# Kernel tuning notes

Measured on AMD Instinct MI355X. Metric: run time of the kernel, lower is better.

Reference implementation:

```python
import jax, jax.numpy as jnp
import numpy as np

N = 50000; E = 800000; B = 500; L = 42
F_IN = 35; HEADS = 10; F_H = 35; F_G = 350
VOCAB = 26; EMB = 128; NF = 16; OUT_DIM = 128; K = 8
NEG_SLOPE = 0.2


def setup_inputs() -> dict:
    key = jax.random.key(0)
    ks = jax.random.split(key, 16)
    inp = {}
    inp['x'] = jax.random.normal(ks[0], (N, F_IN), jnp.float32)
    inp['edge_index'] = jax.random.randint(ks[1], (2, E), 0, N, dtype=jnp.int32)
    inp['batch'] = jnp.sort(jax.random.randint(ks[2], (N,), 0, B, dtype=jnp.int32))
    inp['target'] = jax.random.randint(ks[3], (B, L), 0, VOCAB, dtype=jnp.int32)
    # --- learned parameters ---
    inp['W_gat'] = jax.random.normal(ks[4], (F_IN, HEADS * F_H), jnp.float32) * 0.1
    inp['att_src'] = jax.random.normal(ks[5], (HEADS, F_H), jnp.float32) * 0.1
    inp['att_dst'] = jax.random.normal(ks[6], (HEADS, F_H), jnp.float32) * 0.1
    inp['b_gat'] = jnp.zeros((HEADS * F_H,), jnp.float32)
    inp['W_gcn'] = jax.random.normal(ks[7], (F_G, F_G), jnp.float32) * 0.05
    inp['b_gcn'] = jnp.zeros((F_G,), jnp.float32)
    inp['W_fcg1'] = jax.random.normal(ks[8], (2 * F_G, 1500), jnp.float32) * 0.03
    inp['b_fcg1'] = jnp.zeros((1500,), jnp.float32)
    inp['W_fcg2'] = jax.random.normal(ks[9], (1500, OUT_DIM), jnp.float32) * 0.03
    inp['b_fcg2'] = jnp.zeros((OUT_DIM,), jnp.float32)
    inp['emb_xt'] = jax.random.normal(ks[10], (VOCAB, EMB), jnp.float32) * 0.1
    inp['W_conv'] = jax.random.normal(ks[11], (NF, EMB, K), jnp.float32) * 0.05
    inp['b_conv'] = jnp.zeros((NF,), jnp.float32)
    inp['W_fcxt'] = jax.random.normal(ks[12], (NF * 35, OUT_DIM), jnp.float32) * 0.05
    inp['b_fcxt'] = jnp.zeros((OUT_DIM,), jnp.float32)
    inp['W_fc1'] = jax.random.normal(ks[13], (256, 512), jnp.float32) * 0.05
    inp['b_fc1'] = jnp.zeros((512,), jnp.float32)
    inp['W_out'] = jax.random.normal(ks[14], (512, 1), jnp.float32) * 0.05
    inp['b_out'] = jnp.zeros((1,), jnp.float32)
    return inp


def _add_self_loops(edge_index):
    loop = jnp.arange(N, dtype=edge_index.dtype)
    src = jnp.concatenate([edge_index[0], loop])
    dst = jnp.concatenate([edge_index[1], loop])
    return src, dst


def _gat_conv(x, src, dst, W, att_src, att_dst, b):
    # h: [N, H, C]
    h = (x @ W).reshape(N, HEADS, F_H)
    a_s = jnp.einsum('nhc,hc->nh', h, att_src)  # [N, H]
    a_d = jnp.einsum('nhc,hc->nh', h, att_dst)
    e = jax.nn.leaky_relu(a_s[src] + a_d[dst], NEG_SLOPE)  # [Etot, H]
    # segment softmax over incoming edges per destination node, per head
    m = jax.ops.segment_max(e, dst, num_segments=N)
    m = jnp.where(jnp.isfinite(m), m, 0.0)
    ex = jnp.exp(e - m[dst])
    den = jax.ops.segment_sum(ex, dst, num_segments=N)
    alpha = ex / (den[dst] + 1e-16)  # [Etot, H]
    out = jax.ops.segment_sum(h[src] * alpha[:, :, None], dst, num_segments=N)
    return out.reshape(N, HEADS * F_H) + b, alpha


def _gcn_conv(x, src, dst, W, b):
    deg = jax.ops.segment_sum(jnp.ones_like(dst, jnp.float32), dst, num_segments=N)
    dinv = jnp.where(deg > 0, deg ** -0.5, 0.0)
    norm = dinv[src] * dinv[dst]  # symmetric normalization
    h = x @ W
    return jax.ops.segment_sum(h[src] * norm[:, None], dst, num_segments=N) + b


def reference(x, edge_index, batch, target, W_gat, att_src, att_dst, b_gat,
              W_gcn, b_gcn, W_fcg1, b_fcg1, W_fcg2, b_fcg2, emb_xt,
              W_conv, b_conv, W_fcxt, b_fcxt, W_fc1, b_fc1, W_out, b_out):
    src, dst = _add_self_loops(edge_index)
    # --- graph branch ---
    xg, alpha = _gat_conv(x, src, dst, W_gat, att_src, att_dst, b_gat)
    xg = jax.nn.relu(xg)
    xg = jax.nn.relu(_gcn_conv(xg, src, dst, W_gcn, b_gcn))
    # global max + mean pool per graph
    gmax = jax.ops.segment_max(xg, batch, num_segments=B)
    gsum = jax.ops.segment_sum(xg, batch, num_segments=B)
    cnt = jax.ops.segment_sum(jnp.ones((N,), jnp.float32), batch, num_segments=B)
    gmean = gsum / jnp.maximum(cnt, 1.0)[:, None]
    xg = jnp.concatenate([gmax, gmean], axis=1)  # [B, 700]
    xg = jax.nn.relu(xg @ W_fcg1 + b_fcg1)
    xg = xg @ W_fcg2 + b_fcg2  # [B, 128] (dropout is identity in eval)
    # --- protein branch ---
    emb = emb_xt[target]                      # [B, L, 128]
    emb = jnp.transpose(emb, (0, 2, 1))       # [B, 128, L]
    conv = jax.lax.conv_general_dilated(
        emb, W_conv, window_strides=(1,), padding='VALID',
        dimension_numbers=('NCH', 'OIH', 'NCH'))  # [B, 16, 35]
    conv = conv + b_conv[None, :, None]
    xt = conv.reshape(B, NF * 35)
    xt = xt @ W_fcxt + b_fcxt                 # [B, 128]
    # --- fusion ---
    xc = jnp.concatenate([xg, xt], axis=1)    # [B, 256]
    xc = jax.nn.relu(xc @ W_fc1 + b_fc1)
    out = jax.nn.sigmoid(xc @ W_out + b_out)  # [B, 1]
    return out, alpha
```

## Files before the change

kernel.cpp:

```cpp
#include <hip/hip_runtime.h>
#include <math.h>

#define NN 50000
#define EE 800000
#define BB 500
#define LL 42
#define NHEAD 10
#define FH 35
#define FG 350
#define ETOT (EE + NN)
#define NCHUNK ((NN + 511) / 512)

#define KPAD 384
#define LDH2 352
#define MPAD 50048
#define MB2  512

typedef unsigned short ushort_t;
typedef __attribute__((ext_vector_type(8))) short short8v;
typedef __attribute__((ext_vector_type(4))) float float4v;

__device__ __forceinline__ float lrelu(float x) { return x > 0.f ? x : 0.2f * x; }

__device__ __forceinline__ ushort_t f2bf(float f) {
    unsigned int u = __float_as_uint(f);
    u += 0x7fffu + ((u >> 16) & 1u);
    return (ushort_t)(u >> 16);
}
__device__ __forceinline__ float bflo(unsigned u) { return __uint_as_float(u << 16); }
__device__ __forceinline__ float bfhi(unsigned u) { return __uint_as_float(u & 0xffff0000u); }
__device__ __forceinline__ unsigned packbf(float a, float b) {
    return (unsigned)f2bf(a) | ((unsigned)f2bf(b) << 16);
}

__device__ __forceinline__ void async_cp16(const void* g, void* l) {
    __builtin_amdgcn_global_load_lds((const __attribute__((address_space(1))) unsigned int*)g,
                                     (__attribute__((address_space(3))) unsigned int*)l, 16, 0, 0);
}

__global__ __launch_bounds__(256) void k_init(int* deg, int* cur) {
    int i = blockIdx.x * 256 + threadIdx.x;
    if (i < NN) { deg[i] = 1; cur[i] = 0; }
}

__global__ __launch_bounds__(256) void k_deg(const int* __restrict__ ei, int* deg) {
    int i = blockIdx.x * 256 + threadIdx.x;
    if (i < EE) atomicAdd(&deg[ei[EE + i]], 1);
}

__global__ __launch_bounds__(512) void k_scan1(const int* __restrict__ deg, int* part) {
    int i = blockIdx.x * 512 + threadIdx.x;
    int lane = threadIdx.x & 63, wv = threadIdx.x >> 6;
    int x = (i < NN) ? deg[i] : 0;
    #pragma unroll
    for (int d = 32; d; d >>= 1) x += __shfl_xor(x, d);
    __shared__ int wsum[8];
    if (lane == 0) wsum[wv] = x;
    __syncthreads();
    if (threadIdx.x == 0) {
        int s = 0;
        #pragma unroll
        for (int w = 0; w < 8; w++) s += wsum[w];
        part[blockIdx.x] = s;
    }
}

__global__ __launch_bounds__(64) void k_scan2(const int* __restrict__ part, int* pscan) {
    int l = threadIdx.x;
    int v0 = (l < NCHUNK) ? part[l] : 0;
    #pragma unroll
    for (int d = 1; d < 64; d <<= 1) { int t = __shfl_up(v0, d); if (l >= d) v0 += t; }
    int tot0 = __shfl(v0, 63);
    int v1 = (64 + l < NCHUNK) ? part[64 + l] : 0;
    #pragma unroll
    for (int d = 1; d < 64; d <<= 1) { int t = __shfl_up(v1, d); if (l >= d) v1 += t; }
    v1 += tot0;
    if (l < NCHUNK) pscan[l] = v0;
    if (64 + l < NCHUNK) pscan[64 + l] = v1;
}

__global__ __launch_bounds__(512) void k_scan3(const int* __restrict__ deg, const int* __restrict__ pscan,
                                               int* offs) {
    int i = blockIdx.x * 512 + threadIdx.x;
    int lane = threadIdx.x & 63, wv = threadIdx.x >> 6;
    int x = (i < NN) ? deg[i] : 0;
    int incl = x;
    #pragma unroll
    for (int d = 1; d < 64; d <<= 1) { int t = __shfl_up(incl, d); if (lane >= d) incl += t; }
    __shared__ int wtot[8];
    if (lane == 63) wtot[wv] = incl;
    __syncthreads();
    int woff = 0;
    for (int w = 0; w < wv; w++) woff += wtot[w];
    int base = (blockIdx.x == 0) ? 0 : pscan[blockIdx.x - 1];
    if (i < NN) offs[i] = base + woff + incl - x;
}

__global__ __launch_bounds__(256) void k_scatter(const int* __restrict__ ei, const int* __restrict__ offs,
                                                 int* cur, int* csr_src) {
    int i = blockIdx.x * 256 + threadIdx.x;
    if (i < EE) {
        int s = ei[i], d = ei[EE + i];
        int slot = atomicAdd(&cur[d], 1);
        csr_src[offs[d] + slot] = s;
    } else if (i < ETOT) {
        int v = i - EE;
        int slot = atomicAdd(&cur[v], 1);
        csr_src[offs[v] + slot] = v;
    }
}

__global__ __launch_bounds__(256) void k_dinv(const int* __restrict__ deg, float* dinv) {
    int i = blockIdx.x * 256 + threadIdx.x;
    if (i < NN) dinv[i] = rsqrtf((float)deg[i]);
}

__global__ __launch_bounds__(256) void k_prep_xf(const float* __restrict__ x, ushort_t* __restrict__ xfb) {
    int i = blockIdx.x * 256 + threadIdx.x;
    if (i >= NN * 40) return;
    int n = i / 40, c = i % 40;
    xfb[i] = (c < 35) ? f2bf(x[n * 35 + c]) : (ushort_t)0;
}

__global__ __launch_bounds__(256) void k_prep_att(const float* __restrict__ W_gat, const float* __restrict__ att_s,
                                                  const float* __restrict__ att_d,
                                                  float* __restrict__ wS, float* __restrict__ wD) {
    int i = blockIdx.x * 256 + threadIdx.x;
    if (i >= FG) return;
    int hd = i / 35, c = i % 35;
    float ss = 0.f, dd = 0.f;
    for (int cc = 0; cc < 35; cc++) {
        float w = W_gat[c * FG + hd * 35 + cc];
        ss += w * att_s[hd * 35 + cc];
        dd += w * att_d[hd * 35 + cc];
    }
    wS[i] = ss;
    wD[i] = dd;
}

__global__ __launch_bounds__(256) void k_prep_wbd(const float* __restrict__ W_gat, ushort_t* __restrict__ Wt) {
    int i = blockIdx.x * 256 + threadIdx.x;
    if (i >= KPAD * KPAD) return;
    int n = i / KPAD, k = i % KPAD;
    int hd = k / 36, cc = k % 36;
    float v = 0.f;
    if (n < FG && cc < 35 && hd == n / 35) v = W_gat[cc * FG + n];
    Wt[i] = f2bf(v);
}

__global__ __launch_bounds__(256) void k_prep_wgcn(const float* __restrict__ W, ushort_t* __restrict__ Wt) {
    int i = blockIdx.x * 256 + threadIdx.x;
    if (i >= KPAD * KPAD) return;
    int n = i / KPAD, k = i % KPAD;
    float v = (n < FG && k < FG) ? W[k * FG + n] : 0.f;
    Wt[i] = f2bf(v);
}

__global__ __launch_bounds__(256) void k_prep_w(const float* __restrict__ W, ushort_t* __restrict__ Wt,
                                                int K, int N, int KP, int NP) {
    int i = blockIdx.x * 256 + threadIdx.x;
    if (i >= KP * NP) return;
    int k = i / NP, n = i % NP;
    float v = (k < K && n < N) ? W[(size_t)k * N + n] : 0.f;
    Wt[(size_t)n * KP + k] = f2bf(v);
}

__global__ __launch_bounds__(256) void k_cast_pad(const float* __restrict__ src, ushort_t* __restrict__ dst,
                                                  int M, int K, int MP, int KP) {
    int i = blockIdx.x * 256 + threadIdx.x;
    if (i >= MP * KP) return;
    int r = i / KP, k = i % KP;
    dst[i] = (r < M && k < K) ? f2bf(src[(size_t)r * K + k]) : (ushort_t)0;
}

__global__ __launch_bounds__(256) void k_zero_tail(ushort_t* buf) {
    int i = blockIdx.x * 256 + threadIdx.x;
    int total = (MPAD - NN) * KPAD;
    if (i < total) buf[(size_t)NN * KPAD + i] = 0;
}

__global__ __launch_bounds__(256) void k_mfma(const ushort_t* __restrict__ A, const ushort_t* __restrict__ Bt,
                                              void* __restrict__ C, int M, int Nv, int ldc, int lda,
                                              int ksteps, const float* __restrict__ bias, int act, int bf16out,
                                              int bdiag, int nst) {
    __shared__ ushort_t As[128 * 64];
    __shared__ ushort_t Bs[64 * 64];
    int tid = threadIdx.x;
    int wid = tid >> 6, lane = tid & 63;
    int m0 = blockIdx.y * 128, n0 = blockIdx.x * 64;
    int wm0 = (wid >> 1) * 64, wn0 = (wid & 1) * 32;
    int srow = tid >> 3;
    int scol = (tid & 7) * 8;
    float4v acc[4][2] = {{{0.f,0.f,0.f,0.f},{0.f,0.f,0.f,0.f}},
                         {{0.f,0.f,0.f,0.f},{0.f,0.f,0.f,0.f}},
                         {{0.f,0.f,0.f,0.f},{0.f,0.f,0.f,0.f}},
                         {{0.f,0.f,0.f,0.f},{0.f,0.f,0.f,0.f}}};
    int a_off = (wm0 + (lane & 15)) * 64 + (lane >> 4) * 8;
    int b_off = (wn0 + (lane & 15)) * 64 + (lane >> 4) * 8;
    int ks0 = 0, ks1 = ksteps;
    if (bdiag) {
        int hlo = n0 / 35;
        int hhi = (n0 + 63) / 35; if (hhi > 9) hhi = 9;
        ks0 = (hlo * 36) >> 6;
        ks1 = (hhi * 36 + 36 + 63) >> 6;
    }
    for (int ks = ks0; ks < ks1; ks++) {
        int k0 = ks * 64;
        #pragma unroll
        for (int r = 0; r < 4; r++) {
            const ushort_t* g = A + (size_t)(m0 + r * 32 + srow) * lda + k0 + scol;
            async_cp16(g, As + (r * 256 + tid) * 8);
        }
        #pragma unroll
        for (int r = 0; r < 2; r++) {
            const ushort_t* g = Bt + (size_t)(n0 + r * 32 + srow) * lda + k0 + scol;
            async_cp16(g, Bs + (r * 256 + tid) * 8);
        }
        __syncthreads();
        #pragma unroll
        for (int kh = 0; kh < 2; kh++) {
            short8v b0 = *(const short8v*)&Bs[b_off + kh * 32];
            short8v b1 = *(const short8v*)&Bs[b_off + 16 * 64 + kh * 32];
            #pragma unroll
            for (int mi = 0; mi < 4; mi++) {
                short8v a = *(const short8v*)&As[a_off + mi * 16 * 64 + kh * 32];
                acc[mi][0] = __builtin_amdgcn_mfma_f32_16x16x32_bf16(a, b0, acc[mi][0], 0, 0, 0);
                acc[mi][1] = __builtin_amdgcn_mfma_f32_16x16x32_bf16(a, b1, acc[mi][1], 0, 0, 0);
            }
        }
        __syncthreads();
    }
    int lm = m0 + wm0 + (lane >> 4) * 4;
    int lc = n0 + wn0 + (lane & 15);
    #pragma unroll
    for (int mi = 0; mi < 4; mi++) {
        #pragma unroll
        for (int ni = 0; ni < 2; ni++) {
            int col = lc + ni * 16;
            if (col >= nst) continue;
            float bv = (bias != nullptr && col < Nv) ? bias[col] : 0.f;
            #pragma unroll
            for (int r = 0; r < 4; r++) {
                int row = lm + mi * 16 + r;
                if (row >= M) continue;
                float v = acc[mi][ni][r] + bv;
                if (act) v = fmaxf(v, 0.f);
                if (col >= Nv) v = 0.f;
                if (bf16out) ((ushort_t*)C)[(size_t)row * ldc + col] = f2bf(v);
                else         ((float*)C)[(size_t)row * ldc + col] = v;
            }
        }
    }
}

__global__ __launch_bounds__(256) void k_att2(const float* __restrict__ x, const float* __restrict__ wS,
                                              const float* __restrict__ wD, float* __restrict__ a_s,
                                              float* __restrict__ a_d) {
    int tid = blockIdx.x * 256 + threadIdx.x;
    if (tid >= NN * NHEAD) return;
    int n = tid / NHEAD, hd = tid % NHEAD;
    const float* xr = x + (size_t)n * 35;
    const float* ws = wS + hd * 35;
    const float* wd = wD + hd * 35;
    float as = 0.f, ad = 0.f;
    #pragma unroll
    for (int c = 0; c < 35; c++) { float v = xr[c]; as += v * ws[c]; ad += v * wd[c]; }
    a_s[tid] = as;
    a_d[tid] = ad;
}

__global__ __launch_bounds__(256) void k_gat_agg(const ushort_t* __restrict__ xfb, const float* __restrict__ a_s,
                                                 const float* __restrict__ a_d,
                                                 const int* __restrict__ csr_src,
                                                 const int* __restrict__ offs, const int* __restrict__ deg,
                                                 ushort_t* __restrict__ Zb, float* __restrict__ denArr) {
    int wid = (blockIdx.x * blockDim.x + threadIdx.x) >> 6;
    int lane = threadIdx.x & 63;
    if (wid >= NN) return;
    int o0 = offs[wid], d = deg[wid];
    bool mine = (lane < NHEAD);
    float adv = mine ? a_d[wid * NHEAD + lane] : 0.f;
    int h1 = lane / 18,          c1 = lane % 18;
    int h2 = (lane + 64) / 18,   c2 = (lane + 64) % 18;
    bool g3 = lane < 52;
    int h3 = g3 ? (lane + 128) / 18 : 0;
    int c3 = g3 ? (lane + 128) % 18 : 0;
    float den = 0.f;
    float a1l = 0.f, a1h = 0.f, a2l = 0.f, a2h = 0.f, a3l = 0.f, a3h = 0.f;
    const unsigned* x32 = (const unsigned*)xfb;
    int i = 0;
    for (; i + 2 <= d; i += 2) {
        int s0 = csr_src[o0 + i], s1 = csr_src[o0 + i + 1];
        const unsigned* x0 = x32 + (size_t)s0 * 20;
        const unsigned* x1 = x32 + (size_t)s1 * 20;
        float as0 = mine ? a_s[s0 * NHEAD + lane] : 0.f;
        float as1 = mine ? a_s[s1 * NHEAD + lane] : 0.f;
        unsigned u01 = x0[c1], u02 = x0[c2], u03 = x0[c3];
        unsigned u11 = x1[c1], u12 = x1[c2], u13 = x1[c3];
        float ex0 = __expf(lrelu(as0 + adv));
        float ex1 = __expf(lrelu(as1 + adv));
        den += ex0 + ex1;
        float e01 = __shfl(ex0, h1), e02 = __shfl(ex0, h2), e03 = __shfl(ex0, h3);
        float e11 = __shfl(ex1, h1), e12 = __shfl(ex1, h2), e13 = __shfl(ex1, h3);
        a1l += e01 * bflo(u01) + e11 * bflo(u11);
        a1h += e01 * bfhi(u01) + e11 * bfhi(u11);
        a2l += e02 * bflo(u02) + e12 * bflo(u12);
        a2h += e02 * bfhi(u02) + e12 * bfhi(u12);
        a3l += e03 * bflo(u03) + e13 * bflo(u13);
        a3h += e03 * bfhi(u03) + e13 * bfhi(u13);
    }
    for (; i < d; i++) {
        int s = csr_src[o0 + i];
        const unsigned* x0 = x32 + (size_t)s * 20;
        float as0 = mine ? a_s[s * NHEAD + lane] : 0.f;
        unsigned u01 = x0[c1], u02 = x0[c2], u03 = x0[c3];
        float ex0 = __expf(lrelu(as0 + adv));
        den += ex0;
        float e01 = __shfl(ex0, h1), e02 = __shfl(ex0, h2), e03 = __shfl(ex0, h3);
        a1l += e01 * bflo(u01);  a1h += e01 * bfhi(u01);
        a2l += e02 * bflo(u02);  a2h += e02 * bfhi(u02);
        a3l += e03 * bflo(u03);  a3h += e03 * bfhi(u03);
    }
    float rden = 1.f / (den + 1e-16f);
    if (mine) denArr[wid * NHEAD + lane] = den;
    float r1 = __shfl(rden, h1), r2 = __shfl(rden, h2), r3 = __shfl(rden, h3);
    unsigned* zr = (unsigned*)(Zb + (size_t)wid * KPAD);
    __builtin_nontemporal_store(packbf(a1l * r1, a1h * r1), &zr[lane]);
    __builtin_nontemporal_store(packbf(a2l * r2, a2h * r2), &zr[lane + 64]);
    __builtin_nontemporal_store(g3 ? packbf(a3l * r3, a3h * r3) : 0u, &zr[lane + 128]);
}

__global__ __launch_bounds__(256) void k_alpha(const int* __restrict__ ei, const float* __restrict__ a_s,
                                               const float* __restrict__ a_d, const float* __restrict__ den,
                                               float* __restrict__ alphaOut) {
    int i = blockIdx.x * 256 + threadIdx.x;
    if (i >= ETOT * NHEAD) return;
    int e = i / NHEAD, hd = i % NHEAD;
    int s, dst;
    if (e < EE) { s = ei[e]; dst = ei[EE + e]; }
    else { s = dst = e - EE; }
    float ex = __expf(lrelu(a_s[s * NHEAD + hd] + a_d[dst * NHEAD + hd]));
    __builtin_nontemporal_store(ex / (den[dst * NHEAD + hd] + 1e-16f), &alphaOut[i]);
}

__global__ __launch_bounds__(256) void k_gcn_agg(const ushort_t* __restrict__ h2b,
                                                 const int* __restrict__ csr_src,
                                                 const int* __restrict__ offs, const int* __restrict__ deg,
                                                 const float* __restrict__ dinv, const float* __restrict__ b_gcn,
                                                 float* __restrict__ xg2) {
    int wid = (blockIdx.x * blockDim.x + threadIdx.x) >> 6;
    int lane = threadIdx.x & 63;
    if (wid >= NN) return;
    int o0 = offs[wid], d = deg[wid];
    float wv = dinv[wid];
    bool g3 = lane < 48;
    int w3 = g3 ? (lane + 128) : 0;
    float aL0 = 0.f, aH0 = 0.f, aL1 = 0.f, aH1 = 0.f, aL2 = 0.f, aH2 = 0.f;
    const unsigned* h32 = (const unsigned*)h2b;
    int i = 0;
    for (; i + 2 <= d; i += 2) {
        int s0 = csr_src[o0 + i], s1 = csr_src[o0 + i + 1];
        float w0 = dinv[s0], w1 = dinv[s1];
        const unsigned* h0 = h32 + (size_t)s0 * (LDH2 / 2);
        const unsigned* h1 = h32 + (size_t)s1 * (LDH2 / 2);
        unsigned u00 = h0[lane], u01 = h0[lane + 64], u02 = h0[w3];
        unsigned u10 = h1[lane], u11 = h1[lane + 64], u12 = h1[w3];
        aL0 += w0 * bflo(u00) + w1 * bflo(u10);
        aH0 += w0 * bfhi(u00) + w1 * bfhi(u10);
        aL1 += w0 * bflo(u01) + w1 * bflo(u11);
        aH1 += w0 * bfhi(u01) + w1 * bfhi(u11);
        aL2 += w0 * bflo(u02) + w1 * bflo(u12);
        aH2 += w0 * bfhi(u02) + w1 * bfhi(u12);
    }
    for (; i < d; i++) {
        int s = csr_src[o0 + i];
        float ws = dinv[s];
        const unsigned* hr = h32 + (size_t)s * (LDH2 / 2);
        unsigned u0 = hr[lane], u1 = hr[lane + 64], u2 = hr[w3];
        aL0 += ws * bflo(u0);  aH0 += ws * bfhi(u0);
        aL1 += ws * bflo(u1);  aH1 += ws * bfhi(u1);
        aL2 += ws * bflo(u2);  aH2 += ws * bfhi(u2);
    }
    float* orow = xg2 + (size_t)wid * FG;
    {
        int f = 2 * lane;
        __builtin_nontemporal_store(fmaxf(wv * aL0 + b_gcn[f], 0.f), &orow[f]);
        __builtin_nontemporal_store(fmaxf(wv * aH0 + b_gcn[f + 1], 0.f), &orow[f + 1]);
    }
    {
        int f = 128 + 2 * lane;
        __builtin_nontemporal_store(fmaxf(wv * aL1 + b_gcn[f], 0.f), &orow[f]);
        __builtin_nontemporal_store(fmaxf(wv * aH1 + b_gcn[f + 1], 0.f), &orow[f + 1]);
    }
    {
        int f = 256 + 2 * lane;
        if (f < FG) {
            __builtin_nontemporal_store(fmaxf(wv * aL2 + b_gcn[f], 0.f), &orow[f]);
            __builtin_nontemporal_store(fmaxf(wv * aH2 + b_gcn[f + 1], 0.f), &orow[f + 1]);
        }
    }
}

__device__ __forceinline__ int lowerB(const int* a, int n, int key) {
    int lo = 0, hi = n;
    while (lo < hi) { int mid = (lo + hi) >> 1; if (a[mid] < key) lo = mid + 1; else hi = mid; }
    return lo;
}

__global__ __launch_bounds__(384) void k_pool(const float* __restrict__ xg2, const int* __restrict__ batch,
                                              float* __restrict__ pooled) {
    int g = blockIdx.x;
    int f = threadIdx.x;
    int s = lowerB(batch, NN, g);
    int e = lowerB(batch, NN, g + 1);
    if (f >= FG) return;
    float mx = -INFINITY, sm = 0.f;
    int n = s;
    for (; n + 4 <= e; n += 4) {
        float v0 = xg2[(size_t)(n + 0) * FG + f];
        float v1 = xg2[(size_t)(n + 1) * FG + f];
        float v2 = xg2[(size_t)(n + 2) * FG + f];
        float v3 = xg2[(size_t)(n + 3) * FG + f];
        mx = fmaxf(fmaxf(mx, v0), fmaxf(fmaxf(v1, v2), v3));
        sm += v0 + v1 + v2 + v3;
    }
    for (; n < e; n++) {
        float v = xg2[(size_t)n * FG + f];
        mx = fmaxf(mx, v);
        sm += v;
    }
    int cnt = e - s;
    pooled[g * 700 + f] = mx;
    pooled[g * 700 + FG + f] = sm / fmaxf((float)cnt, 1.f);
}

__global__ __launch_bounds__(256) void k_conv(const int* __restrict__ target, const float* __restrict__ emb,
                                              const float* __restrict__ Wc, const float* __restrict__ bc,
                                              float* __restrict__ xt) {
    __shared__ float embL[26 * 132];
    __shared__ float WL[16 * 8 * 128];
    __shared__ int   tgL[2 * LL];
    int tid = threadIdx.x;
    int b0 = blockIdx.x * 2;
    for (int i = tid; i < 26 * 128; i += 256) {
        int r = i >> 7, e = i & 127;
        embL[r * 132 + e] = emb[i];
    }
    for (int i = tid; i < 16384; i += 256) {
        int f = i >> 10, rem = i & 1023, k = rem >> 7, e = rem & 127;
        WL[i] = Wc[f * 1024 + e * 8 + k];
    }
    if (tid < 2 * LL) tgL[tid] = target[b0 * LL + tid];
    __syncthreads();
    #pragma unroll
    for (int pass = 0; pass < 2; pass++) {
        int r = tid + pass * 256;
        if (r >= 280) break;
        int bl = r / 140, rem = r % 140;
        int fq = rem / 35, t = rem % 35;
        const int* tg = &tgL[bl * LL];
        float ac0 = 0.f, ac1 = 0.f, ac2 = 0.f, ac3 = 0.f;
        for (int k = 0; k < 8; k++) {
            const float* er = &embL[tg[t + k] * 132];
            const float* w0 = &WL[((fq * 4 + 0) * 8 + k) * 128];
            const float* w1 = &WL[((fq * 4 + 1) * 8 + k) * 128];
            const float* w2 = &WL[((fq * 4 + 2) * 8 + k) * 128];
            const float* w3 = &WL[((fq * 4 + 3) * 8 + k) * 128];
            #pragma unroll 8
            for (int e = 0; e < 128; e += 4) {
                float4 a = *(const float4*)&er[e];
                float4 q0 = *(const float4*)&w0[e];
                float4 q1 = *(const float4*)&w1[e];
                float4 q2 = *(const float4*)&w2[e];
                float4 q3 = *(const float4*)&w3[e];
                ac0 += a.x * q0.x + a.y * q0.y + a.z * q0.z + a.w * q0.w;
                ac1 += a.x * q1.x + a.y * q1.y + a.z * q1.z + a.w * q1.w;
                ac2 += a.x * q2.x + a.y * q2.y + a.z * q2.z + a.w * q2.w;
                ac3 += a.x * q3.x + a.y * q3.y + a.z * q3.z + a.w * q3.w;
            }
        }
        int b = b0 + bl, fb = fq * 4;
        xt[b * 560 + (fb + 0) * 35 + t] = ac0 + bc[fb + 0];
        xt[b * 560 + (fb + 1) * 35 + t] = ac1 + bc[fb + 1];
        xt[b * 560 + (fb + 2) * 35 + t] = ac2 + bc[fb + 2];
        xt[b * 560 + (fb + 3) * 35 + t] = ac3 + bc[fb + 3];
    }
}

__global__ __launch_bounds__(256) void k_out(const float* __restrict__ f1, const float* __restrict__ W_out,
                                             const float* __restrict__ b_out, float* __restrict__ out) {
    int wid = (blockIdx.x * blockDim.x + threadIdx.x) >> 6;
    int lane = threadIdx.x & 63;
    if (wid >= BB) return;
    const float* xr = f1 + (size_t)wid * 512;
    float acc = 0.f;
    #pragma unroll
    for (int k = 0; k < 8; k++) acc += xr[lane + k * 64] * W_out[lane + k * 64];
    #pragma unroll
    for (int d = 32; d; d >>= 1) acc += __shfl_xor(acc, d);
    if (lane == 0) out[wid] = 1.f / (1.f + __expf(-(acc + b_out[0])));
}

extern "C" void kernel_launch(void* const* d_in, const int* in_sizes, int n_in,
                              void* d_out, int out_size, void* d_ws, size_t ws_size,
                              hipStream_t stream) {
    const float* x      = (const float*)d_in[0];
    const int*   ei     = (const int*)d_in[1];
    const int*   batch  = (const int*)d_in[2];
    const int*   target = (const int*)d_in[3];
    const float* W_gat  = (const float*)d_in[4];
    const float* att_s  = (const float*)d_in[5];
    const float* att_d  = (const float*)d_in[6];
    const float* b_gat  = (const float*)d_in[7];
    const float* W_gcn  = (const float*)d_in[8];
    const float* b_gcn  = (const float*)d_in[9];
    const float* W_fcg1 = (const float*)d_in[10];
    const float* b_fcg1 = (const float*)d_in[11];
    const float* W_fcg2 = (const float*)d_in[12];
    const float* b_fcg2 = (const float*)d_in[13];
    const float* embxt  = (const float*)d_in[14];
    const float* W_conv = (const float*)d_in[15];
    const float* b_conv = (const float*)d_in[16];
    const float* W_fcxt = (const float*)d_in[17];
    const float* b_fcxt = (const float*)d_in[18];
    const float* W_fc1  = (const float*)d_in[19];
    const float* b_fc1  = (const float*)d_in[20];
    const float* W_out  = (const float*)d_in[21];
    const float* b_out  = (const float*)d_in[22];

    float* out_sig  = (float*)d_out;
    float* alphaOut = (float*)d_out + BB;

    size_t o = 0;
    auto alloc = [&](size_t bytes) -> void* {
        o = (o + 255) & ~(size_t)255;
        void* p = (char*)d_ws + o;
        o += bytes;
        return p;
    };
    int*   deg     = (int*)alloc((size_t)NN * 4);
    int*   cur     = (int*)alloc((size_t)NN * 4);
    int*   offs    = (int*)alloc((size_t)NN * 4);
    int*   part    = (int*)alloc(128 * 4);
    int*   pscan   = (int*)alloc(128 * 4);
    int*   csr_src = (int*)alloc((size_t)ETOT * 4);
    float* dinv    = (float*)alloc((size_t)NN * 4);
    float* a_s     = (float*)alloc((size_t)NN * NHEAD * 4);
    float* a_d     = (float*)alloc((size_t)NN * NHEAD * 4);
    float* denArr  = (float*)alloc((size_t)NN * NHEAD * 4);
    ushort_t* xfb  = (ushort_t*)alloc((size_t)NN * 40 * 2);
    float* wS      = (float*)alloc((size_t)FG * 4);
    float* wD      = (float*)alloc((size_t)FG * 4);
    ushort_t* WtBD = (ushort_t*)alloc((size_t)KPAD * KPAD * 2);
    ushort_t* WtGC = (ushort_t*)alloc((size_t)KPAD * KPAD * 2);
    ushort_t* WtF1 = (ushort_t*)alloc((size_t)1536 * 704 * 2);
    ushort_t* WtF2 = (ushort_t*)alloc((size_t)128 * 1536 * 2);
    ushort_t* WtFX = (ushort_t*)alloc((size_t)128 * 576 * 2);
    ushort_t* WtFC = (ushort_t*)alloc((size_t)512 * 256 * 2);
    float* pooled  = (float*)alloc((size_t)BB * 700 * 4);
    ushort_t* pooledb = (ushort_t*)alloc((size_t)MB2 * 704 * 2);
    ushort_t* t1b  = (ushort_t*)alloc((size_t)MB2 * 1536 * 2);
    float* xt      = (float*)alloc((size_t)BB * 560 * 4);
    ushort_t* xtb  = (ushort_t*)alloc((size_t)MB2 * 576 * 2);
    ushort_t* xcb  = (ushort_t*)alloc((size_t)MB2 * 256 * 2);
    float* f1      = (float*)alloc((size_t)MB2 * 512 * 4);
    ushort_t* hb   = (ushort_t*)alloc((size_t)MPAD * KPAD * 2);
    char*  R2      = (char*)alloc((size_t)NN * FG * 4);
    ushort_t* xg1b = (ushort_t*)R2;
    float* xg2     = (float*)R2;
    (void)ws_size; (void)n_in; (void)in_sizes; (void)out_size;

    auto mfma = [&](const ushort_t* A, const ushort_t* Bt, void* C, const float* bias,
                    int M2, int Nv, int NP, int ldc, int KP, int act, int bf16out, int bdiag, int nst) {
        dim3 g(NP / 64, M2 / 128);
        k_mfma<<<g, 256, 0, stream>>>(A, Bt, C, M2, Nv, ldc, KP, KP / 64, bias, act, bf16out, bdiag, nst);
    };

    k_init<<<(NN + 255) / 256, 256, 0, stream>>>(deg, cur);
    k_deg<<<(EE + 255) / 256, 256, 0, stream>>>(ei, deg);
    k_scan1<<<NCHUNK, 512, 0, stream>>>(deg, part);
    k_scan2<<<1, 64, 0, stream>>>(part, pscan);
    k_scan3<<<NCHUNK, 512, 0, stream>>>(deg, pscan, offs);
    k_scatter<<<(ETOT + 255) / 256, 256, 0, stream>>>(ei, offs, cur, csr_src);
    k_dinv<<<(NN + 255) / 256, 256, 0, stream>>>(deg, dinv);

    k_prep_xf<<<(NN * 40 + 255) / 256, 256, 0, stream>>>(x, xfb);
    k_prep_att<<<2, 256, 0, stream>>>(W_gat, att_s, att_d, wS, wD);
    k_prep_wbd<<<(KPAD * KPAD + 255) / 256, 256, 0, stream>>>(W_gat, WtBD);
    k_prep_wgcn<<<(KPAD * KPAD + 255) / 256, 256, 0, stream>>>(W_gcn, WtGC);
    k_prep_w<<<(704 * 1536 + 255) / 256, 256, 0, stream>>>(W_fcg1, WtF1, 700, 1500, 704, 1536);
    k_prep_w<<<(1536 * 128 + 255) / 256, 256, 0, stream>>>(W_fcg2, WtF2, 1500, 128, 1536, 128);
    k_prep_w<<<(576 * 128 + 255) / 256, 256, 0, stream>>>(W_fcxt, WtFX, 560, 128, 576, 128);
    k_prep_w<<<(256 * 512 + 255) / 256, 256, 0, stream>>>(W_fc1, WtFC, 256, 512, 256, 512);
    k_zero_tail<<<((MPAD - NN) * KPAD + 255) / 256, 256, 0, stream>>>(hb);

    k_att2<<<(NN * NHEAD + 255) / 256, 256, 0, stream>>>(x, wS, wD, a_s, a_d);
    k_gat_agg<<<(NN + 3) / 4, 256, 0, stream>>>(xfb, a_s, a_d, csr_src, offs, deg, hb, denArr);
    k_alpha<<<(ETOT * NHEAD + 255) / 256, 256, 0, stream>>>(ei, a_s, a_d, denArr, alphaOut);
    mfma(hb, WtBD, xg1b, b_gat, MPAD, FG, KPAD, KPAD, KPAD, 1, 1, 1, KPAD);

    mfma(xg1b, WtGC, hb, nullptr, MPAD, FG, KPAD, LDH2, KPAD, 0, 1, 0, LDH2);
    k_gcn_agg<<<(NN + 3) / 4, 256, 0, stream>>>(hb, csr_src, offs, deg, dinv, b_gcn, xg2);

    k_pool<<<BB, 384, 0, stream>>>(xg2, batch, pooled);
    k_cast_pad<<<(MB2 * 704 + 255) / 256, 256, 0, stream>>>(pooled, pooledb, BB, 700, MB2, 704);
    mfma(pooledb, WtF1, t1b, b_fcg1, MB2, 1500, 1536, 1536, 704, 1, 1, 0, 1536);
    mfma(t1b, WtF2, xcb, b_fcg2, MB2, 128, 128, 256, 1536, 0, 1, 0, 128);
    k_conv<<<250, 256, 0, stream>>>(target, embxt, W_conv, b_conv, xt);
    k_cast_pad<<<(MB2 * 576 + 255) / 256, 256, 0, stream>>>(xt, xtb, BB, 560, MB2, 576);
    mfma(xtb, WtFX, xcb + 128, b_fcxt, MB2, 128, 128, 256, 576, 0, 1, 0, 128);
    mfma(xcb, WtFC, f1, b_fc1, MB2, 512, 512, 512, 256, 1, 0, 0, 512);
    k_out<<<(BB + 3) / 4, 256, 0, stream>>>(f1, W_out, b_out, out_sig);
}
```

Measured before the change: 605.0 us.

## Fuse node prep with attention scores, unroll aggregations, store GCN output as bf16

Merges the bf16 feature cast and the per-node attention-score computation into one kernel that reads x once. It also unrolls both edge-aggregation loops to four neighbours per step and shrinks their blocks to two waves. The GCN aggregation now writes bf16 instead of fp32, which halves the write traffic and the read traffic of the pooling kernel that follows. In exchange, the pooled max and mean inputs lose precision to bf16 rounding.

```diff
diff --git a/kernel.cpp b/kernel.cpp
--- a/kernel.cpp
+++ b/kernel.cpp
@@ -115,13 +115,6 @@
     if (i < NN) dinv[i] = rsqrtf((float)deg[i]);
 }
 
-__global__ __launch_bounds__(256) void k_prep_xf(const float* __restrict__ x, ushort_t* __restrict__ xfb) {
-    int i = blockIdx.x * 256 + threadIdx.x;
-    if (i >= NN * 40) return;
-    int n = i / 40, c = i % 40;
-    xfb[i] = (c < 35) ? f2bf(x[n * 35 + c]) : (ushort_t)0;
-}
-
 __global__ __launch_bounds__(256) void k_prep_att(const float* __restrict__ W_gat, const float* __restrict__ att_s,
                                                   const float* __restrict__ att_d,
                                                   float* __restrict__ wS, float* __restrict__ wD) {
@@ -136,6 +129,35 @@
     }
     wS[i] = ss;
     wD[i] = dd;
+}
+
+__global__ __launch_bounds__(256) void k_prep_node(const float* __restrict__ x, const float* __restrict__ wS,
+                                                   const float* __restrict__ wD, ushort_t* __restrict__ xfb,
+                                                   float* __restrict__ a_s, float* __restrict__ a_d) {
+    __shared__ float sw[FG], dw[FG];
+    int tid = threadIdx.x;
+    for (int i = tid; i < FG; i += 256) { sw[i] = wS[i]; dw[i] = wD[i]; }
+    __syncthreads();
+    int n = blockIdx.x * 256 + tid;
+    if (n >= NN) return;
+    float xr[35];
+    #pragma unroll
+    for (int c = 0; c < 35; c++) xr[c] = x[(size_t)n * 35 + c];
+    unsigned* xo = (unsigned*)(xfb + (size_t)n * 40);
+    #pragma unroll
+    for (int w = 0; w < 17; w++) xo[w] = packbf(xr[2 * w], xr[2 * w + 1]);
+    xo[17] = packbf(xr[34], 0.f);
+    xo[18] = 0u; xo[19] = 0u;
+    #pragma unroll
+    for (int hd = 0; hd < NHEAD; hd++) {
+        const float* ws = &sw[hd * 35];
+        const float* wd = &dw[hd * 35];
+        float as = 0.f, ad = 0.f;
+        #pragma unroll
+        for (int c = 0; c < 35; c++) { float v = xr[c]; as += v * ws[c]; ad += v * wd[c]; }
+        a_s[n * NHEAD + hd] = as;
+        a_d[n * NHEAD + hd] = ad;
+    }
 }
 
 __global__ __launch_bounds__(256) void k_prep_wbd(const float* __restrict__ W_gat, ushort_t* __restrict__ Wt) {
@@ -253,28 +275,12 @@
     }
 }
 
-__global__ __launch_bounds__(256) void k_att2(const float* __restrict__ x, const float* __restrict__ wS,
-                                              const float* __restrict__ wD, float* __restrict__ a_s,
-                                              float* __restrict__ a_d) {
-    int tid = blockIdx.x * 256 + threadIdx.x;
-    if (tid >= NN * NHEAD) return;
-    int n = tid / NHEAD, hd = tid % NHEAD;
-    const float* xr = x + (size_t)n * 35;
-    const float* ws = wS + hd * 35;
-    const float* wd = wD + hd * 35;
-    float as = 0.f, ad = 0.f;
-    #pragma unroll
-    for (int c = 0; c < 35; c++) { float v = xr[c]; as += v * ws[c]; ad += v * wd[c]; }
-    a_s[tid] = as;
-    a_d[tid] = ad;
-}
-
-__global__ __launch_bounds__(256) void k_gat_agg(const ushort_t* __restrict__ xfb, const float* __restrict__ a_s,
+__global__ __launch_bounds__(128) void k_gat_agg(const ushort_t* __restrict__ xfb, const float* __restrict__ a_s,
                                                  const float* __restrict__ a_d,
                                                  const int* __restrict__ csr_src,
                                                  const int* __restrict__ offs, const int* __restrict__ deg,
                                                  ushort_t* __restrict__ Zb, float* __restrict__ denArr) {
-    int wid = (blockIdx.x * blockDim.x + threadIdx.x) >> 6;
+    int wid = blockIdx.x * 2 + (threadIdx.x >> 6);
     int lane = threadIdx.x & 63;
     if (wid >= NN) return;
     int o0 = offs[wid], d = deg[wid];
@@ -289,25 +295,36 @@
     float a1l = 0.f, a1h = 0.f, a2l = 0.f, a2h = 0.f, a3l = 0.f, a3h = 0.f;
     const unsigned* x32 = (const unsigned*)xfb;
     int i = 0;
-    for (; i + 2 <= d; i += 2) {
-        int s0 = csr_src[o0 + i], s1 = csr_src[o0 + i + 1];
+    for (; i + 4 <= d; i += 4) {
+        int s0 = csr_src[o0 + i],     s1 = csr_src[o0 + i + 1];
+        int s2 = csr_src[o0 + i + 2], s3 = csr_src[o0 + i + 3];
         const unsigned* x0 = x32 + (size_t)s0 * 20;
         const unsigned* x1 = x32 + (size_t)s1 * 20;
+        const unsigned* x2 = x32 + (size_t)s2 * 20;
+        const unsigned* x3 = x32 + (size_t)s3 * 20;
         float as0 = mine ? a_s[s0 * NHEAD + lane] : 0.f;
         float as1 = mine ? a_s[s1 * NHEAD + lane] : 0.f;
+        float as2 = mine ? a_s[s2 * NHEAD + lane] : 0.f;
+        float as3 = mine ? a_s[s3 * NHEAD + lane] : 0.f;
         unsigned u01 = x0[c1], u02 = x0[c2], u03 = x0[c3];
         unsigned u11 = x1[c1], u12 = x1[c2], u13 = x1[c3];
+        unsigned u21 = x2[c1], u22 = x2[c2], u23 = x2[c3];
+        unsigned u31 = x3[c1], u32 = x3[c2], u33 = x3[c3];
         float ex0 = __expf(lrelu(as0 + adv));
         float ex1 = __expf(lrelu(as1 + adv));
-        den += ex0 + ex1;
+        float ex2 = __expf(lrelu(as2 + adv));
+        float ex3 = __expf(lrelu(as3 + adv));
+        den += (ex0 + ex1) + (ex2 + ex3);
         float e01 = __shfl(ex0, h1), e02 = __shfl(ex0, h2), e03 = __shfl(ex0, h3);
         float e11 = __shfl(ex1, h1), e12 = __shfl(ex1, h2), e13 = __shfl(ex1, h3);
-        a1l += e01 * bflo(u01) + e11 * bflo(u11);
-        a1h += e01 * bfhi(u01) + e11 * bfhi(u11);
-        a2l += e02 * bflo(u02) + e12 * bflo(u12);
-        a2h += e02 * bfhi(u02) + e12 * bfhi(u12);
-        a3l += e03 * bflo(u03) + e13 * bflo(u13);
-        a3h += e03 * bfhi(u03) + e13 * bfhi(u13);
+        float e21 = __shfl(ex2, h1), e22 = __shfl(ex2, h2), e23 = __shfl(ex2, h3);
+        float e31 = __shfl(ex3, h1), e32 = __shfl(ex3, h2), e33 = __shfl(ex3, h3);
+        a1l += e01 * bflo(u01) + e11 * bflo(u11) + e21 * bflo(u21) + e31 * bflo(u31);
+        a1h += e01 * bfhi(u01) + e11 * bfhi(u11) + e21 * bfhi(u21) + e31 * bfhi(u31);
+        a2l += e02 * bflo(u02) + e12 * bflo(u12) + e22 * bflo(u22) + e32 * bflo(u32);
+        a2h += e02 * bfhi(u02) + e12 * bfhi(u12) + e22 * bfhi(u22) + e32 * bfhi(u32);
+        a3l += e03 * bflo(u03) + e13 * bflo(u13) + e23 * bflo(u23) + e33 * bflo(u33);
+        a3h += e03 * bfhi(u03) + e13 * bfhi(u13) + e23 * bfhi(u23) + e33 * bfhi(u33);
     }
     for (; i < d; i++) {
         int s = csr_src[o0 + i];
@@ -343,12 +360,12 @@
     __builtin_nontemporal_store(ex / (den[dst * NHEAD + hd] + 1e-16f), &alphaOut[i]);
 }
 
-__global__ __launch_bounds__(256) void k_gcn_agg(const ushort_t* __restrict__ h2b,
+__global__ __launch_bounds__(128) void k_gcn_agg(const ushort_t* __restrict__ h2b,
                                                  const int* __restrict__ csr_src,
                                                  const int* __restrict__ offs, const int* __restrict__ deg,
                                                  const float* __restrict__ dinv, const float* __restrict__ b_gcn,
-                                                 float* __restrict__ xg2) {
-    int wid = (blockIdx.x * blockDim.x + threadIdx.x) >> 6;
+                                                 ushort_t* __restrict__ xg2b) {
+    int wid = blockIdx.x * 2 + (threadIdx.x >> 6);
     int lane = threadIdx.x & 63;
     if (wid >= NN) return;
     int o0 = offs[wid], d = deg[wid];
@@ -358,19 +375,24 @@
     float aL0 = 0.f, aH0 = 0.f, aL1 = 0.f, aH1 = 0.f, aL2 = 0.f, aH2 = 0.f;
     const unsigned* h32 = (const unsigned*)h2b;
     int i = 0;
-    for (; i + 2 <= d; i += 2) {
-        int s0 = csr_src[o0 + i], s1 = csr_src[o0 + i + 1];
-        float w0 = dinv[s0], w1 = dinv[s1];
+    for (; i + 4 <= d; i += 4) {
+        int s0 = csr_src[o0 + i],     s1 = csr_src[o0 + i + 1];
+        int s2 = csr_src[o0 + i + 2], s3 = csr_src[o0 + i + 3];
+        float q0 = dinv[s0], q1 = dinv[s1], q2 = dinv[s2], q3 = dinv[s3];
         const unsigned* h0 = h32 + (size_t)s0 * (LDH2 / 2);
         const unsigned* h1 = h32 + (size_t)s1 * (LDH2 / 2);
+        const unsigned* h2 = h32 + (size_t)s2 * (LDH2 / 2);
+        const unsigned* h3 = h32 + (size_t)s3 * (LDH2 / 2);
         unsigned u00 = h0[lane], u01 = h0[lane + 64], u02 = h0[w3];
         unsigned u10 = h1[lane], u11 = h1[lane + 64], u12 = h1[w3];
-        aL0 += w0 * bflo(u00) + w1 * bflo(u10);
-        aH0 += w0 * bfhi(u00) + w1 * bfhi(u10);
-        aL1 += w0 * bflo(u01) + w1 * bflo(u11);
-        aH1 += w0 * bfhi(u01) + w1 * bfhi(u11);
-        aL2 += w0 * bflo(u02) + w1 * bflo(u12);
-        aH2 += w0 * bfhi(u02) + w1 * bfhi(u12);
+        unsigned u20 = h2[lane], u21 = h2[lane + 64], u22 = h2[w3];
+        unsigned u30 = h3[lane], u31 = h3[lane + 64], u32 = h3[w3];
+        aL0 += q0 * bflo(u00) + q1 * bflo(u10) + q2 * bflo(u20) + q3 * bflo(u30);
+        aH0 += q0 * bfhi(u00) + q1 * bfhi(u10) + q2 * bfhi(u20) + q3 * bfhi(u30);
+        aL1 += q0 * bflo(u01) + q1 * bflo(u11) + q2 * bflo(u21) + q3 * bflo(u31);
+        aH1 += q0 * bfhi(u01) + q1 * bfhi(u11) + q2 * bfhi(u21) + q3 * bfhi(u31);
+        aL2 += q0 * bflo(u02) + q1 * bflo(u12) + q2 * bflo(u22) + q3 * bflo(u32);
+        aH2 += q0 * bfhi(u02) + q1 * bfhi(u12) + q2 * bfhi(u22) + q3 * bfhi(u32);
     }
     for (; i < d; i++) {
         int s = csr_src[o0 + i];
@@ -381,23 +403,21 @@
         aL1 += ws * bflo(u1);  aH1 += ws * bfhi(u1);
         aL2 += ws * bflo(u2);  aH2 += ws * bfhi(u2);
     }
-    float* orow = xg2 + (size_t)wid * FG;
+    unsigned* orow = (unsigned*)(xg2b + (size_t)wid * FG);
     {
         int f = 2 * lane;
-        __builtin_nontemporal_store(fmaxf(wv * aL0 + b_gcn[f], 0.f), &orow[f]);
-        __builtin_nontemporal_store(fmaxf(wv * aH0 + b_gcn[f + 1], 0.f), &orow[f + 1]);
+        __builtin_nontemporal_store(packbf(fmaxf(wv * aL0 + b_gcn[f], 0.f),
+                                           fmaxf(wv * aH0 + b_gcn[f + 1], 0.f)), &orow[lane]);
     }
     {
         int f = 128 + 2 * lane;
-        __builtin_nontemporal_store(fmaxf(wv * aL1 + b_gcn[f], 0.f), &orow[f]);
-        __builtin_nontemporal_store(fmaxf(wv * aH1 + b_gcn[f + 1], 0.f), &orow[f + 1]);
-    }
-    {
+        __builtin_nontemporal_store(packbf(fmaxf(wv * aL1 + b_gcn[f], 0.f),
+                                           fmaxf(wv * aH1 + b_gcn[f + 1], 0.f)), &orow[64 + lane]);
+    }
+    if (lane < 47) {
         int f = 256 + 2 * lane;
-        if (f < FG) {
-            __builtin_nontemporal_store(fmaxf(wv * aL2 + b_gcn[f], 0.f), &orow[f]);
-            __builtin_nontemporal_store(fmaxf(wv * aH2 + b_gcn[f + 1], 0.f), &orow[f + 1]);
-        }
+        __builtin_nontemporal_store(packbf(fmaxf(wv * aL2 + b_gcn[f], 0.f),
+                                           fmaxf(wv * aH2 + b_gcn[f + 1], 0.f)), &orow[128 + lane]);
     }
 }
 
@@ -407,31 +427,38 @@
     return lo;
 }
 
-__global__ __launch_bounds__(384) void k_pool(const float* __restrict__ xg2, const int* __restrict__ batch,
+__global__ __launch_bounds__(256) void k_pool(const ushort_t* __restrict__ xg2b, const int* __restrict__ batch,
                                               float* __restrict__ pooled) {
     int g = blockIdx.x;
-    int f = threadIdx.x;
+    int w = threadIdx.x;
+    if (w >= 175) return;
     int s = lowerB(batch, NN, g);
     int e = lowerB(batch, NN, g + 1);
-    if (f >= FG) return;
-    float mx = -INFINITY, sm = 0.f;
+    const unsigned* base = (const unsigned*)xg2b;
+    float mx0 = -INFINITY, mx1 = -INFINITY, sm0 = 0.f, sm1 = 0.f;
     int n = s;
-    for (; n + 4 <= e; n += 4) {
-        float v0 = xg2[(size_t)(n + 0) * FG + f];
-        float v1 = xg2[(size_t)(n + 1) * FG + f];
-        float v2 = xg2[(size_t)(n + 2) * FG + f];
-        float v3 = xg2[(size_t)(n + 3) * FG + f];
-        mx = fmaxf(fmaxf(mx, v0), fmaxf(fmaxf(v1, v2), v3));
-        sm += v0 + v1 + v2 + v3;
+    for (; n + 2 <= e; n += 2) {
+        unsigned ua = base[(size_t)n * 175 + w];
+        unsigned ub = base[(size_t)(n + 1) * 175 + w];
+        float a0 = bflo(ua), a1 = bfhi(ua), b0 = bflo(ub), b1 = bfhi(ub);
+        mx0 = fmaxf(mx0, fmaxf(a0, b0));
+        mx1 = fmaxf(mx1, fmaxf(a1, b1));
+        sm0 += a0 + b0;
+        sm1 += a1 + b1;
     }
     for (; n < e; n++) {
-        float v = xg2[(size_t)n * FG + f];
-        mx = fmaxf(mx, v);
-        sm += v;
-    }
-    int cnt = e - s;
-    pooled[g * 700 + f] = mx;
-    pooled[g * 700 + FG + f] = sm / fmaxf((float)cnt, 1.f);
+        unsigned ua = base[(size_t)n * 175 + w];
+        float a0 = bflo(ua), a1 = bfhi(ua);
+        mx0 = fmaxf(mx0, a0);
+        mx1 = fmaxf(mx1, a1);
+        sm0 += a0;
+        sm1 += a1;
+    }
+    float rc = 1.f / fmaxf((float)(e - s), 1.f);
+    pooled[g * 700 + 2 * w]       = mx0;
+    pooled[g * 700 + 2 * w + 1]   = mx1;
+    pooled[g * 700 + FG + 2 * w]     = sm0 * rc;
+    pooled[g * 700 + FG + 2 * w + 1] = sm1 * rc;
 }
 
 __global__ __launch_bounds__(256) void k_conv(const int* __restrict__ target, const float* __restrict__ emb,
@@ -567,7 +594,7 @@
     ushort_t* hb   = (ushort_t*)alloc((size_t)MPAD * KPAD * 2);
     char*  R2      = (char*)alloc((size_t)NN * FG * 4);
     ushort_t* xg1b = (ushort_t*)R2;
-    float* xg2     = (float*)R2;
+    ushort_t* xg2b = (ushort_t*)R2;
     (void)ws_size; (void)n_in; (void)in_sizes; (void)out_size;
 
     auto mfma = [&](const ushort_t* A, const ushort_t* Bt, void* C, const float* bias,
@@ -584,8 +611,8 @@
     k_scatter<<<(ETOT + 255) / 256, 256, 0, stream>>>(ei, offs, cur, csr_src);
     k_dinv<<<(NN + 255) / 256, 256, 0, stream>>>(deg, dinv);
 
-    k_prep_xf<<<(NN * 40 + 255) / 256, 256, 0, stream>>>(x, xfb);
     k_prep_att<<<2, 256, 0, stream>>>(W_gat, att_s, att_d, wS, wD);
+    k_prep_node<<<(NN + 255) / 256, 256, 0, stream>>>(x, wS, wD, xfb, a_s, a_d);
     k_prep_wbd<<<(KPAD * KPAD + 255) / 256, 256, 0, stream>>>(W_gat, WtBD);
     k_prep_wgcn<<<(KPAD * KPAD + 255) / 256, 256, 0, stream>>>(W_gcn, WtGC);
     k_prep_w<<<(704 * 1536 + 255) / 256, 256, 0, stream>>>(W_fcg1, WtF1, 700, 1500, 704, 1536);
@@ -594,15 +621,14 @@
     k_prep_w<<<(256 * 512 + 255) / 256, 256, 0, stream>>>(W_fc1, WtFC, 256, 512, 256, 512);
     k_zero_tail<<<((MPAD - NN) * KPAD + 255) / 256, 256, 0, stream>>>(hb);
 
-    k_att2<<<(NN * NHEAD + 255) / 256, 256, 0, stream>>>(x, wS, wD, a_s, a_d);
-    k_gat_agg<<<(NN + 3) / 4, 256, 0, stream>>>(xfb, a_s, a_d, csr_src, offs, deg, hb, denArr);
+    k_gat_agg<<<(NN + 1) / 2, 128, 0, stream>>>(xfb, a_s, a_d, csr_src, offs, deg, hb, denArr);
     k_alpha<<<(ETOT * NHEAD + 255) / 256, 256, 0, stream>>>(ei, a_s, a_d, denArr, alphaOut);
     mfma(hb, WtBD, xg1b, b_gat, MPAD, FG, KPAD, KPAD, KPAD, 1, 1, 1, KPAD);
 
     mfma(xg1b, WtGC, hb, nullptr, MPAD, FG, KPAD, LDH2, KPAD, 0, 1, 0, LDH2);
-    k_gcn_agg<<<(NN + 3) / 4, 256, 0, stream>>>(hb, csr_src, offs, deg, dinv, b_gcn, xg2);
-
-    k_pool<<<BB, 384, 0, stream>>>(xg2, batch, pooled);
+    k_gcn_agg<<<(NN + 1) / 2, 128, 0, stream>>>(hb, csr_src, offs, deg, dinv, b_gcn, xg2b);
+
+    k_pool<<<BB, 256, 0, stream>>>(xg2b, batch, pooled);
     k_cast_pad<<<(MB2 * 704 + 255) / 256, 256, 0, stream>>>(pooled, pooledb, BB, 700, MB2, 704);
     mfma(pooledb, WtF1, t1b, b_fcg1, MB2, 1500, 1536, 1536, 704, 1, 1, 0, 1536);
     mfma(t1b, WtF2, xcb, b_fcg2, MB2, 128, 128, 256, 1536, 0, 1, 0, 128);
```

New measurement: 582.9 us. 1.04x faster.
